# Optimization experiments

Hardware: AMD Instinct MI355X
Metric: run time of the kernel (lower is better)

## Reference

```python
import jax, jax.numpy as jnp
import numpy as np
from jax import lax

EPS = 1e-5  # BatchNorm eps (eval mode, running stats)
HEADS = 8

# --- surrogate-gradient Heaviside (sigmoid surrogate, alpha=4) ---
@jax.custom_vjp
def spike(u):
    return (u >= 0.0).astype(u.dtype)

def _spike_fwd(u):
    return spike(u), u

def _spike_bwd(u, g):
    s = jax.nn.sigmoid(4.0 * u)
    return (g * 4.0 * s * (1.0 - s),)

spike.defvjp(_spike_fwd, _spike_bwd)

def lif(x, tau=0.5, threshold=1.0):
    """Multi-step LIF over leading time axis: v_t = tau*v_{t-1} + x_t,
    s_t = H(v_t - threshold), hard reset v_t *= (1 - s_t)."""
    def step(v, xt):
        v = tau * v + xt
        s = spike(v - threshold)
        return v * (1.0 - s), s
    _, out = lax.scan(step, jnp.zeros_like(x[0]), x)
    return out

def bn_eval(x, gamma, beta, mean, var):
    # x: (T,B,C,N); per-channel affine using running stats
    inv = gamma / jnp.sqrt(var + EPS)
    return x * inv[None, None, :, None] + (beta - mean * inv)[None, None, :, None]

def setup_inputs() -> dict:
    key = jax.random.key(0)
    ks = jax.random.split(key, 12)
    T, B, C, H, W = 4, 32, 384, 16, 16
    d = {}
    d['x'] = jax.random.normal(ks[0], (T, B, C, H, W), dtype=jnp.float32)
    # 1x1 Conv1d weights == (C_out, C_in) matrices
    sc = 1.0 / np.sqrt(C)
    d['q_w'] = jax.random.normal(ks[1], (C, C), dtype=jnp.float32) * sc
    d['q_gamma'] = jnp.ones((C,), jnp.float32)
    d['q_beta'] = jnp.zeros((C,), jnp.float32)
    d['q_mean'] = jax.random.normal(ks[2], (C,), dtype=jnp.float32) * 0.1
    d['q_var'] = jax.random.uniform(ks[3], (C,), dtype=jnp.float32) + 0.5
    d['k_w'] = jax.random.normal(ks[4], (C, C), dtype=jnp.float32) * sc
    d['k_gamma'] = jnp.ones((C,), jnp.float32)
    d['k_beta'] = jnp.zeros((C,), jnp.float32)
    d['k_mean'] = jax.random.normal(ks[5], (C,), dtype=jnp.float32) * 0.1
    d['k_var'] = jax.random.uniform(ks[6], (C,), dtype=jnp.float32) + 0.5
    d['proj_w'] = jax.random.normal(ks[7], (C, C), dtype=jnp.float32) * sc
    d['proj_b'] = jax.random.normal(ks[8], (C,), dtype=jnp.float32) * 0.01
    d['proj_gamma'] = jnp.ones((C,), jnp.float32)
    d['proj_beta'] = jnp.zeros((C,), jnp.float32)
    d['proj_mean'] = jax.random.normal(ks[9], (C,), dtype=jnp.float32) * 0.1
    d['proj_var'] = jax.random.uniform(ks[10], (C,), dtype=jnp.float32) + 0.5
    d['mem_alpha'] = jnp.float32(0.2)
    return d

def reference(x, q_w, q_gamma, q_beta, q_mean, q_var,
              k_w, k_gamma, k_beta, k_mean, k_var,
              proj_w, proj_b, proj_gamma, proj_beta, proj_mean, proj_var,
              mem_alpha):
    T, B, C, H, W = x.shape
    Hh = HEADS
    Dh = C // Hh
    N = H * W
    # proj_lif applied to raw input, then flatten spatial dims
    s = lif(x, tau=0.5, threshold=1.0).reshape(T, B, C, N)
    # q path: 1x1 conv (channel GEMM) -> BN -> LIF
    q = lif(bn_eval(jnp.einsum('tbcn,dc->tbdn', s, q_w), q_gamma, q_beta, q_mean, q_var),
            tau=0.5, threshold=1.0).reshape(T, B, Hh, Dh, N)
    # k path
    k = lif(bn_eval(jnp.einsum('tbcn,dc->tbdn', s, k_w), k_gamma, k_beta, k_mean, k_var),
            tau=0.5, threshold=1.0).reshape(T, B, Hh, Dh, N)
    # temporal decayed memory: m_0 = q_0; m_t = alpha*m_{t-1} + (1-alpha)*q_{t-1}
    def mstep(m_prev, q_prev):
        m = mem_alpha * m_prev + (1.0 - mem_alpha) * q_prev
        return m, m
    _, mems_rest = lax.scan(mstep, q[0], q[:-1])
    mems = jnp.concatenate([q[:1], mems_rest], axis=0)  # (T,B,Hh,Dh,N)
    # cat along Dh then sum == sum(mems)+sum(q)
    q_sum = jnp.sum(mems, axis=3, keepdims=True) + jnp.sum(q, axis=3, keepdims=True)
    attn = lif(q_sum, tau=0.5, threshold=0.5)  # (T,B,Hh,1,N)
    y = (attn * k).reshape(T, B, C, N)
    # proj conv (with bias) -> BN -> reshape back to (T,B,C,H,W)
    y = jnp.einsum('tbcn,dc->tbdn', y, proj_w) + proj_b[None, None, :, None]
    y = bn_eval(y, proj_gamma, proj_beta, proj_mean, proj_var)
    return y.reshape(T, B, C, H, W)
```

## Files before the change

### kernel.cpp

```cpp
#include <hip/hip_runtime.h>

#define T_ 4
#define B_ 32
#define C_ 384
#define N_ 256
#define HEADS_ 8
#define DH_ 48
#define EPS_ 1e-5f
#define NW_ (C_*C_)

typedef _Float16 f16;
typedef __attribute__((ext_vector_type(8))) _Float16 f16x8;
typedef __attribute__((ext_vector_type(16))) float f32x16;

#define PSCALE     4096.0f
#define PSCALE_INV (1.0f/4096.0f)
#define SPIKE_BYTE 0x3Cu

__device__ __forceinline__ void unpack4(unsigned int w, unsigned int& lo, unsigned int& hi) {
#if defined(__has_builtin) && __has_builtin(__builtin_amdgcn_perm)
    lo = __builtin_amdgcn_perm(w, w, 0x010C000Cu);
    hi = __builtin_amdgcn_perm(w, w, 0x030C020Cu);
#else
    lo = ((w & 0xFFu) << 8) | ((w & 0xFF00u) << 16);
    hi = ((w & 0x00FF0000u) >> 8) | (w & 0xFF000000u);
#endif
}

__device__ __forceinline__ void unpack16(uint4 w, uint4& o0, uint4& o1) {
    unpack4(w.x, o0.x, o0.y); unpack4(w.y, o0.z, o0.w);
    unpack4(w.z, o1.x, o1.y); unpack4(w.w, o1.z, o1.w);
}

__global__ __launch_bounds__(256)
void prep_kernel(const float* __restrict__ x, unsigned char* __restrict__ s,
                 const float* __restrict__ qw, const float* __restrict__ kw,
                 const float* __restrict__ pw,
                 f16* __restrict__ q2, f16* __restrict__ k2, f16* __restrict__ p2)
{
    if (blockIdx.z == 32) {
        const int base = (blockIdx.y * 4 + blockIdx.x) * 256 + threadIdx.x;
        int idx = base;
#pragma unroll 4
        for (int it = 0; it < 48; ++it) {
            {
                float w = qw[idx]; f16 a = (f16)w; f16 bb = (f16)((w - (float)a) * PSCALE);
                q2[idx] = a; q2[NW_ + idx] = bb;
            }
            {
                float w = kw[idx]; f16 a = (f16)w; f16 bb = (f16)((w - (float)a) * PSCALE);
                k2[idx] = a; k2[NW_ + idx] = bb;
            }
            {
                float w = pw[idx]; f16 a = (f16)w; f16 bb = (f16)((w - (float)a) * PSCALE);
                p2[idx] = a; p2[NW_ + idx] = bb;
            }
            idx += 3072;
        }
        return;
    }

    const int tid = threadIdx.x;
    const int ng = tid & 15;
    const int cg = tid >> 4;
    const int n4 = blockIdx.x * 64 + ng * 4;
    const int c0 = blockIdx.y * 128 + cg * 8;
    const int b  = blockIdx.z;

    float v[8][4];
#pragma unroll
    for (int i = 0; i < 8; ++i)
#pragma unroll
        for (int j = 0; j < 4; ++j) v[i][j] = 0.f;

#pragma unroll
    for (int t = 0; t < T_; ++t) {
        const float* xt = x + (((size_t)t * B_ + b) * C_) * N_;
        float4 xv[8];
#pragma unroll
        for (int i = 0; i < 8; ++i)
            xv[i] = *(const float4*)&xt[(size_t)(c0 + i) * N_ + n4];
#pragma unroll
        for (int j = 0; j < 4; ++j) {
            union { unsigned char bb[8]; uint2 u; } u;
#pragma unroll
            for (int i = 0; i < 8; ++i) {
                float xa = (j == 0) ? xv[i].x : (j == 1) ? xv[i].y
                         : (j == 2) ? xv[i].z : xv[i].w;
                float vv = 0.5f * v[i][j] + xa;
                int sp = (vv >= 1.0f) ? 1 : 0;
                v[i][j] = sp ? 0.f : vv;
                u.bb[i] = sp ? (unsigned char)SPIKE_BYTE : (unsigned char)0;
            }
            unsigned char* dst = s + (((size_t)t * B_ + b) * N_ + n4 + j) * (size_t)C_ + c0;
            *(uint2*)dst = u.u;
        }
    }
}

__global__ __launch_bounds__(256)
void qk_gemm_lif_kernel(const f16* __restrict__ Wq, const f16* __restrict__ Wk,
                        const unsigned char* __restrict__ S,
                        const float* __restrict__ qg, const float* __restrict__ qb,
                        const float* __restrict__ qm, const float* __restrict__ qv,
                        const float* __restrict__ kg, const float* __restrict__ kb,
                        const float* __restrict__ km, const float* __restrict__ kv,
                        unsigned char* __restrict__ q_spk,
                        unsigned char* __restrict__ k_spk)
{
    __shared__ __align__(16) char smem[36864];
    f16 (*As)[72]      = reinterpret_cast<f16(*)[72]>(smem);
    f16 (*Bs)[64][72]  = reinterpret_cast<f16(*)[64][72]>(smem + 18432);

    const int tid  = threadIdx.x;
    const int lane = tid & 63;
    const int wave = tid >> 6;
    const int wm = wave & 1, wd = wave >> 1;
    const int l31 = lane & 31;
    const int lhi = lane >> 5;

    const int mb = blockIdx.x;
    const int b  = mb >> 3;
    const int n0 = (mb & 7) * 32;
    const int dp0 = blockIdx.y * 64;
    const int path = (dp0 >= C_) ? 1 : 0;
    const int d0 = dp0 - path * C_;

    const f16* W = path ? Wk : Wq;
    const float* g_  = path ? kg : qg;
    const float* be_ = path ? kb : qb;
    const float* m_  = path ? km : qm;
    const float* va_ = path ? kv : qv;
    unsigned char* spk = path ? k_spk : q_spk;

    const int dcol = d0 + wd * 32 + l31;
    const float inv = g_[dcol] / sqrtf(va_[dcol] + EPS_);
    const float add = be_[dcol] - m_[dcol] * inv;

    const int ar = tid >> 1;
    const int ah = (tid & 1) * 32;
    const int at = ar >> 5;
    const int anl = ar & 31;
    const unsigned char* arow = S + (((size_t)at * B_ + b) * N_ + n0 + anl) * (size_t)C_;
    const int aps = 4 * anl + ((at + (anl >> 1)) & 3);

    const int bp = tid >> 7;
    const int brr = (tid >> 1) & 63;
    const int bh = (tid & 1) * 32;
    const f16* brow = W + (size_t)bp * NW_ + (size_t)(d0 + brr) * C_;

    const int abase = 4 * (l31 >> 2) + ((l31 + (l31 >> 3)) & 3);
    const f16* pa0 = &As[wm * 64 + abase][0];
    const f16* pa1 = pa0 + 32 * 72;

    f32x16 acc[2][2];
#pragma unroll
    for (int ms = 0; ms < 2; ++ms)
#pragma unroll
        for (int p = 0; p < 2; ++p)
#pragma unroll
            for (int r = 0; r < 16; ++r) acc[ms][p][r] = 0.f;

    uint4 ra0 = *(const uint4*)(arow + ah);
    uint4 ra1 = *(const uint4*)(arow + ah + 16);
    uint4 rb0 = *(const uint4*)(brow + bh);
    uint4 rb1 = *(const uint4*)(brow + bh + 8);
    uint4 rb2 = *(const uint4*)(brow + bh + 16);
    uint4 rb3 = *(const uint4*)(brow + bh + 24);

#pragma unroll
    for (int ic = 0; ic < 6; ++ic) {
        __syncthreads();
        {
            uint4 o0, o1;
            unpack16(ra0, o0, o1);
            *(uint4*)&As[aps][ah]      = o0;
            *(uint4*)&As[aps][ah + 8]  = o1;
            unpack16(ra1, o0, o1);
            *(uint4*)&As[aps][ah + 16] = o0;
            *(uint4*)&As[aps][ah + 24] = o1;
            *(uint4*)&Bs[bp][brr][bh]      = rb0;
            *(uint4*)&Bs[bp][brr][bh + 8]  = rb1;
            *(uint4*)&Bs[bp][brr][bh + 16] = rb2;
            *(uint4*)&Bs[bp][brr][bh + 24] = rb3;
        }
        __syncthreads();
        if (ic < 5) {
            const int kn = ic * 64 + 64;
            ra0 = *(const uint4*)(arow + kn + ah);
            ra1 = *(const uint4*)(arow + kn + ah + 16);
            rb0 = *(const uint4*)(brow + kn + bh);
            rb1 = *(const uint4*)(brow + kn + bh + 8);
            rb2 = *(const uint4*)(brow + kn + bh + 16);
            rb3 = *(const uint4*)(brow + kn + bh + 24);
        }
#pragma unroll
        for (int kk = 0; kk < 4; ++kk) {
            const int ko = kk * 16 + lhi * 8;
            f16x8 a0 = *(const f16x8*)(pa0 + ko);
            f16x8 a1 = *(const f16x8*)(pa1 + ko);
            f16x8 b0 = *(const f16x8*)&Bs[0][wd * 32 + l31][ko];
            f16x8 b1 = *(const f16x8*)&Bs[1][wd * 32 + l31][ko];
            acc[0][0] = __builtin_amdgcn_mfma_f32_32x32x16_f16(a0, b0, acc[0][0], 0, 0, 0);
            acc[1][0] = __builtin_amdgcn_mfma_f32_32x32x16_f16(a1, b0, acc[1][0], 0, 0, 0);
            acc[0][1] = __builtin_amdgcn_mfma_f32_32x32x16_f16(a0, b1, acc[0][1], 0, 0, 0);
            acc[1][1] = __builtin_amdgcn_mfma_f32_32x32x16_f16(a1, b1, acc[1][1], 0, 0, 0);
        }
    }

#pragma unroll
    for (int ms = 0; ms < 2; ++ms)
#pragma unroll
    for (int g = 0; g < 4; ++g) {
        const int n = n0 + wm * 16 + ms * 8 + 2 * g + lhi;
        float v = 0.f;
#pragma unroll
        for (int t = 0; t < 4; ++t) {
            const int r = g * 4 + t;
            float val = (acc[ms][0][r] + acc[ms][1][r] * PSCALE_INV) * inv + add;
            float vv = 0.5f * v + val;
            int sp = (vv >= 1.0f) ? 1 : 0;
            v = sp ? 0.f : vv;
            spk[(((size_t)t * B_ + b) * N_ + n) * C_ + dcol] =
                sp ? (unsigned char)SPIKE_BYTE : (unsigned char)0;
        }
    }
}

__global__ __launch_bounds__(256)
void head_attn_kernel(const unsigned char* __restrict__ q_spk,
                      const float* __restrict__ alpha_p,
                      unsigned char* __restrict__ attn)
{
    int i = blockIdx.x * 256 + threadIdx.x;
    int n = i & (N_ - 1);
    int h = (i >> 8) & (HEADS_ - 1);
    int b = i >> 11;
    const float alpha = alpha_p[0];
    const int stride = B_ * HEADS_ * N_;
    float M = 0.f, v = 0.f, Sprev = 0.f;
#pragma unroll
    for (int t = 0; t < T_; ++t) {
        const uint4* p = (const uint4*)(q_spk + (((size_t)(t * B_ + b) * N_) + n) * C_ + h * DH_);
        int cnt = 0;
#pragma unroll
        for (int j = 0; j < 3; ++j) {
            uint4 w = p[j];
            cnt += __popc(w.x & 0x04040404u) + __popc(w.y & 0x04040404u)
                 + __popc(w.z & 0x04040404u) + __popc(w.w & 0x04040404u);
        }
        float Sqt = (float)cnt;
        if (t == 0) M = Sqt;
        else        M = alpha * M + (1.f - alpha) * Sprev;
        float qsum = M + Sqt;
        float vv = 0.5f * v + qsum;
        unsigned char sp = (vv >= 0.5f) ? 1 : 0;
        v = sp ? 0.f : vv;
        attn[(size_t)t * stride + i] = sp;
        Sprev = Sqt;
    }
}

__global__ __launch_bounds__(256)
void proj_gemm_kernel(const f16* __restrict__ Wp,
                      const unsigned char* __restrict__ K8,
                      const unsigned char* __restrict__ attn,
                      const float* __restrict__ bias,
                      const float* __restrict__ gamma, const float* __restrict__ beta,
                      const float* __restrict__ mean,  const float* __restrict__ var,
                      float* __restrict__ out)
{
    __shared__ __align__(16) char smem[36864];
    f16 (*As)[72]     = reinterpret_cast<f16(*)[72]>(smem);
    f16 (*Bs)[64][72] = reinterpret_cast<f16(*)[64][72]>(smem + 18432);

    const int tid  = threadIdx.x;
    const int lane = tid & 63;
    const int wave = tid >> 6;
    const int wm = wave & 1, wd = wave >> 1;
    const int l31 = lane & 31;
    const int lhi = lane >> 5;

    const int mb = blockIdx.x;
    const int tb = mb >> 1;
    const int n0 = (mb & 1) * 128;
    const int d0 = blockIdx.y * 64;

    const int dcol = d0 + wd * 32 + l31;
    const float iv = gamma[dcol] / sqrtf(var[dcol] + EPS_);
    const float ad = beta[dcol] - mean[dcol] * iv + bias[dcol] * iv;

    const int ar = tid >> 1;
    const int ah = (tid & 1) * 32;
    const int an = n0 + ar;
    const unsigned char* arow = K8 + ((size_t)tb * N_ + an) * (size_t)C_;
    const unsigned char* At = attn + (size_t)tb * HEADS_ * N_;

    const int bp = tid >> 7;
    const int brr = (tid >> 1) & 63;
    const int bh = (tid & 1) * 32;
    const f16* brow = Wp + (size_t)bp * NW_ + (size_t)(d0 + brr) * C_;

    f32x16 acc[2][2];
#pragma unroll
    for (int ms = 0; ms < 2; ++ms)
#pragma unroll
        for (int p = 0; p < 2; ++p)
#pragma unroll
            for (int r = 0; r < 16; ++r) acc[ms][p][r] = 0.f;

    uint2 wa0, wa1, wa2, wa3;
    unsigned char am0, am1, am2, am3;
    uint4 rb0, rb1, rb2, rb3;
    {
        const int c0 = ah;
        am0 = At[(size_t)((c0     ) / DH_) * N_ + an]; wa0 = *(const uint2*)(arow + c0);
        am1 = At[(size_t)((c0 +  8) / DH_) * N_ + an]; wa1 = *(const uint2*)(arow + c0 + 8);
        am2 = At[(size_t)((c0 + 16) / DH_) * N_ + an]; wa2 = *(const uint2*)(arow + c0 + 16);
        am3 = At[(size_t)((c0 + 24) / DH_) * N_ + an]; wa3 = *(const uint2*)(arow + c0 + 24);
        rb0 = *(const uint4*)(brow + bh);
        rb1 = *(const uint4*)(brow + bh + 8);
        rb2 = *(const uint4*)(brow + bh + 16);
        rb3 = *(const uint4*)(brow + bh + 24);
    }

#pragma unroll
    for (int ic = 0; ic < 6; ++ic) {
        __syncthreads();
        {
            uint2 w;
            uint4 o;
            w = am0 ? wa0 : make_uint2(0u, 0u);
            unpack4(w.x, o.x, o.y); unpack4(w.y, o.z, o.w);
            *(uint4*)&As[ar][ah] = o;
            w = am1 ? wa1 : make_uint2(0u, 0u);
            unpack4(w.x, o.x, o.y); unpack4(w.y, o.z, o.w);
            *(uint4*)&As[ar][ah + 8] = o;
            w = am2 ? wa2 : make_uint2(0u, 0u);
            unpack4(w.x, o.x, o.y); unpack4(w.y, o.z, o.w);
            *(uint4*)&As[ar][ah + 16] = o;
            w = am3 ? wa3 : make_uint2(0u, 0u);
            unpack4(w.x, o.x, o.y); unpack4(w.y, o.z, o.w);
            *(uint4*)&As[ar][ah + 24] = o;
            *(uint4*)&Bs[bp][brr][bh]      = rb0;
            *(uint4*)&Bs[bp][brr][bh + 8]  = rb1;
            *(uint4*)&Bs[bp][brr][bh + 16] = rb2;
            *(uint4*)&Bs[bp][brr][bh + 24] = rb3;
        }
        __syncthreads();
        if (ic < 5) {
            const int kn = ic * 64 + 64;
            const int c0 = kn + ah;
            am0 = At[(size_t)((c0     ) / DH_) * N_ + an]; wa0 = *(const uint2*)(arow + c0);
            am1 = At[(size_t)((c0 +  8) / DH_) * N_ + an]; wa1 = *(const uint2*)(arow + c0 + 8);
            am2 = At[(size_t)((c0 + 16) / DH_) * N_ + an]; wa2 = *(const uint2*)(arow + c0 + 16);
            am3 = At[(size_t)((c0 + 24) / DH_) * N_ + an]; wa3 = *(const uint2*)(arow + c0 + 24);
            rb0 = *(const uint4*)(brow + kn + bh);
            rb1 = *(const uint4*)(brow + kn + bh + 8);
            rb2 = *(const uint4*)(brow + kn + bh + 16);
            rb3 = *(const uint4*)(brow + kn + bh + 24);
        }
#pragma unroll
        for (int kk = 0; kk < 4; ++kk) {
            const int ko = kk * 16 + lhi * 8;
            f16x8 a0 = *(const f16x8*)&As[wm * 64 + l31][ko];
            f16x8 a1 = *(const f16x8*)&As[wm * 64 + 32 + l31][ko];
            f16x8 b0 = *(const f16x8*)&Bs[0][wd * 32 + l31][ko];
            f16x8 b1 = *(const f16x8*)&Bs[1][wd * 32 + l31][ko];
            acc[0][0] = __builtin_amdgcn_mfma_f32_32x32x16_f16(a0, b0, acc[0][0], 0, 0, 0);
            acc[1][0] = __builtin_amdgcn_mfma_f32_32x32x16_f16(a1, b0, acc[1][0], 0, 0, 0);
            acc[0][1] = __builtin_amdgcn_mfma_f32_32x32x16_f16(a0, b1, acc[0][1], 0, 0, 0);
            acc[1][1] = __builtin_amdgcn_mfma_f32_32x32x16_f16(a1, b1, acc[1][1], 0, 0, 0);
        }
    }

    float* obase = out + ((size_t)tb * C_ + dcol) * N_;
#pragma unroll
    for (int ms = 0; ms < 2; ++ms)
#pragma unroll
    for (int r = 0; r < 16; ++r) {
        int n = n0 + wm * 64 + ms * 32 + (r & 3) + 8 * (r >> 2) + 4 * lhi;
        float val = acc[ms][0][r] + acc[ms][1][r] * PSCALE_INV;
        obase[n] = val * iv + ad;
    }
}

extern "C" void kernel_launch(void* const* d_in, const int* in_sizes, int n_in,
                              void* d_out, int out_size, void* d_ws, size_t ws_size,
                              hipStream_t stream)
{
    const float* x       = (const float*)d_in[0];
    const float* q_w     = (const float*)d_in[1];
    const float* q_gamma = (const float*)d_in[2];
    const float* q_beta  = (const float*)d_in[3];
    const float* q_mean  = (const float*)d_in[4];
    const float* q_var   = (const float*)d_in[5];
    const float* k_w     = (const float*)d_in[6];
    const float* k_gamma = (const float*)d_in[7];
    const float* k_beta  = (const float*)d_in[8];
    const float* k_mean  = (const float*)d_in[9];
    const float* k_var   = (const float*)d_in[10];
    const float* proj_w  = (const float*)d_in[11];
    const float* proj_b  = (const float*)d_in[12];
    const float* p_gamma = (const float*)d_in[13];
    const float* p_beta  = (const float*)d_in[14];
    const float* p_mean  = (const float*)d_in[15];
    const float* p_var   = (const float*)d_in[16];
    const float* m_alpha = (const float*)d_in[17];

    float* out = (float*)d_out;

    const size_t SPK_BYTES = (size_t)T_ * B_ * N_ * C_;
    const size_t W2_BYTES  = (size_t)2 * NW_ * sizeof(f16);
    const size_t TBHN      = (size_t)T_ * B_ * HEADS_ * N_;

    unsigned char* ws = (unsigned char*)d_ws;
    size_t off = 0;
    auto carve = [&](size_t bytes) {
        off = (off + 255) & ~(size_t)255;
        void* p = ws + off;
        off += bytes;
        return p;
    };
    unsigned char* s_u8  = (unsigned char*)carve(SPK_BYTES);
    unsigned char* q_spk = (unsigned char*)carve(SPK_BYTES);
    unsigned char* k_spk = (unsigned char*)carve(SPK_BYTES);
    f16* Wq2    = (f16*)carve(W2_BYTES);
    f16* Wk2    = (f16*)carve(W2_BYTES);
    f16* Wp2    = (f16*)carve(W2_BYTES);
    unsigned char* attn = (unsigned char*)carve(TBHN);

    dim3 pgrid1(4, 3, 33);
    prep_kernel<<<pgrid1, 256, 0, stream>>>(x, s_u8, q_w, k_w, proj_w,
                                            Wq2, Wk2, Wp2);

    dim3 qkgrid(256, 12);
    qk_gemm_lif_kernel<<<qkgrid, 256, 0, stream>>>(Wq2, Wk2, s_u8,
                                                   q_gamma, q_beta, q_mean, q_var,
                                                   k_gamma, k_beta, k_mean, k_var,
                                                   q_spk, k_spk);

    head_attn_kernel<<<(B_ * HEADS_ * N_) / 256, 256, 0, stream>>>(q_spk, m_alpha, attn);

    dim3 pjgrid(256, 6);
    proj_gemm_kernel<<<pjgrid, 256, 0, stream>>>(Wp2, k_spk, attn, proj_b,
                                                 p_gamma, p_beta, p_mean, p_var, out);
}
```

Measured before the change: 212.6 us.

## Double-buffer LDS tiles in QK GEMM with halved K-chunk

The QK GEMM+LIF kernel now uses two LDS buffers with a K-chunk of 32 instead of one buffer with a K-chunk of 64. Global loads for the next chunk are issued before the MFMAs on the current buffer and written to the other buffer afterwards, so only one barrier is needed per iteration. The aim is to overlap LDS stores and global loads with compute and to drop the second __syncthreads. In exchange it runs twice as many iterations and barriers, uses slightly more LDS, and the 40-element row pitch may cause LDS bank conflicts.

After: 211.5 us. About the same (-0.5%).

```diff
diff --git a/kernel.cpp b/kernel.cpp
--- a/kernel.cpp
+++ b/kernel.cpp
@@ -108,9 +108,13 @@
                         unsigned char* __restrict__ q_spk,
                         unsigned char* __restrict__ k_spk)
 {
-    __shared__ __align__(16) char smem[36864];
-    f16 (*As)[72]      = reinterpret_cast<f16(*)[72]>(smem);
-    f16 (*Bs)[64][72]  = reinterpret_cast<f16(*)[64][72]>(smem + 18432);
+    __shared__ __align__(16) char smem[40960];
+    f16 (*Ab[2])[40];
+    f16 (*Bb[2])[64][40];
+    Ab[0] = reinterpret_cast<f16(*)[40]>(smem);
+    Ab[1] = reinterpret_cast<f16(*)[40]>(smem + 10240);
+    Bb[0] = reinterpret_cast<f16(*)[64][40]>(smem + 20480);
+    Bb[1] = reinterpret_cast<f16(*)[64][40]>(smem + 30720);
 
     const int tid  = threadIdx.x;
     const int lane = tid & 63;
@@ -137,21 +141,22 @@
     const float inv = g_[dcol] / sqrtf(va_[dcol] + EPS_);
     const float add = be_[dcol] - m_[dcol] * inv;
 
-    const int ar = tid >> 1;
-    const int ah = (tid & 1) * 32;
-    const int at = ar >> 5;
+    const int ar  = tid >> 1;
+    const int ah  = (tid & 1) * 16;
+    const int at  = ar >> 5;
     const int anl = ar & 31;
     const unsigned char* arow = S + (((size_t)at * B_ + b) * N_ + n0 + anl) * (size_t)C_;
     const int aps = 4 * anl + ((at + (anl >> 1)) & 3);
 
-    const int bp = tid >> 7;
-    const int brr = (tid >> 1) & 63;
-    const int bh = (tid & 1) * 32;
+    const int rb  = tid >> 1;
+    const int bp  = rb >> 6;
+    const int brr = rb & 63;
+    const int bh  = (tid & 1) * 16;
     const f16* brow = W + (size_t)bp * NW_ + (size_t)(d0 + brr) * C_;
 
     const int abase = 4 * (l31 >> 2) + ((l31 + (l31 >> 3)) & 3);
-    const f16* pa0 = &As[wm * 64 + abase][0];
-    const f16* pa1 = pa0 + 32 * 72;
+    const int ard0 = wm * 64 + abase;
+    const int brd  = wd * 32 + l31;
 
     f32x16 acc[2][2];
 #pragma unroll
@@ -161,50 +166,47 @@
 #pragma unroll
             for (int r = 0; r < 16; ++r) acc[ms][p][r] = 0.f;
 
-    uint4 ra0 = *(const uint4*)(arow + ah);
-    uint4 ra1 = *(const uint4*)(arow + ah + 16);
-    uint4 rb0 = *(const uint4*)(brow + bh);
-    uint4 rb1 = *(const uint4*)(brow + bh + 8);
-    uint4 rb2 = *(const uint4*)(brow + bh + 16);
-    uint4 rb3 = *(const uint4*)(brow + bh + 24);
-
-#pragma unroll
-    for (int ic = 0; ic < 6; ++ic) {
+    uint4 la  = *(const uint4*)(arow + ah);
+    uint4 lb0 = *(const uint4*)(brow + bh);
+    uint4 lb1 = *(const uint4*)(brow + bh + 8);
+    {
+        uint4 o0, o1;
+        unpack16(la, o0, o1);
+        *(uint4*)&Ab[0][aps][ah]     = o0;
+        *(uint4*)&Ab[0][aps][ah + 8] = o1;
+        *(uint4*)&Bb[0][bp][brr][bh]     = lb0;
+        *(uint4*)&Bb[0][bp][brr][bh + 8] = lb1;
+    }
+
+#pragma unroll
+    for (int ic = 0; ic < 12; ++ic) {
+        const int cur = ic & 1, nxt = cur ^ 1;
         __syncthreads();
-        {
-            uint4 o0, o1;
-            unpack16(ra0, o0, o1);
-            *(uint4*)&As[aps][ah]      = o0;
-            *(uint4*)&As[aps][ah + 8]  = o1;
-            unpack16(ra1, o0, o1);
-            *(uint4*)&As[aps][ah + 16] = o0;
-            *(uint4*)&As[aps][ah + 24] = o1;
-            *(uint4*)&Bs[bp][brr][bh]      = rb0;
-            *(uint4*)&Bs[bp][brr][bh + 8]  = rb1;
-            *(uint4*)&Bs[bp][brr][bh + 16] = rb2;
-            *(uint4*)&Bs[bp][brr][bh + 24] = rb3;
-        }
-        __syncthreads();
-        if (ic < 5) {
-            const int kn = ic * 64 + 64;
-            ra0 = *(const uint4*)(arow + kn + ah);
-            ra1 = *(const uint4*)(arow + kn + ah + 16);
-            rb0 = *(const uint4*)(brow + kn + bh);
-            rb1 = *(const uint4*)(brow + kn + bh + 8);
-            rb2 = *(const uint4*)(brow + kn + bh + 16);
-            rb3 = *(const uint4*)(brow + kn + bh + 24);
-        }
-#pragma unroll
-        for (int kk = 0; kk < 4; ++kk) {
+        if (ic < 11) {
+            const int kn = (ic + 1) * 32;
+            la  = *(const uint4*)(arow + kn + ah);
+            lb0 = *(const uint4*)(brow + kn + bh);
+            lb1 = *(const uint4*)(brow + kn + bh + 8);
+        }
+#pragma unroll
+        for (int kk = 0; kk < 2; ++kk) {
             const int ko = kk * 16 + lhi * 8;
-            f16x8 a0 = *(const f16x8*)(pa0 + ko);
-            f16x8 a1 = *(const f16x8*)(pa1 + ko);
-            f16x8 b0 = *(const f16x8*)&Bs[0][wd * 32 + l31][ko];
-            f16x8 b1 = *(const f16x8*)&Bs[1][wd * 32 + l31][ko];
+            f16x8 a0 = *(const f16x8*)&Ab[cur][ard0][ko];
+            f16x8 a1 = *(const f16x8*)&Ab[cur][ard0 + 32][ko];
+            f16x8 b0 = *(const f16x8*)&Bb[cur][0][brd][ko];
+            f16x8 b1 = *(const f16x8*)&Bb[cur][1][brd][ko];
             acc[0][0] = __builtin_amdgcn_mfma_f32_32x32x16_f16(a0, b0, acc[0][0], 0, 0, 0);
             acc[1][0] = __builtin_amdgcn_mfma_f32_32x32x16_f16(a1, b0, acc[1][0], 0, 0, 0);
             acc[0][1] = __builtin_amdgcn_mfma_f32_32x32x16_f16(a0, b1, acc[0][1], 0, 0, 0);
             acc[1][1] = __builtin_amdgcn_mfma_f32_32x32x16_f16(a1, b1, acc[1][1], 0, 0, 0);
+        }
+        if (ic < 11) {
+            uint4 o0, o1;
+            unpack16(la, o0, o1);
+            *(uint4*)&Ab[nxt][aps][ah]     = o0;
+            *(uint4*)&Ab[nxt][aps][ah + 8] = o1;
+            *(uint4*)&Bb[nxt][bp][brr][bh]     = lb0;
+            *(uint4*)&Bb[nxt][bp][brr][bh + 8] = lb1;
         }
     }
 
```
